# Optimization experiments

Hardware: AMD Instinct MI355X
Metric: run time of the kernel (lower is better)

The kernel has to match this reference:

```python
import jax, jax.numpy as jnp
import numpy as np

H, LMAX, NSEG, EPS = 8, 2, 16, 1e-7
S = (LMAX + 1) ** 2  # 9 spherical components
L_OF_M = jnp.asarray(np.floor(np.sqrt(np.arange(S))).astype(np.int32))  # degree l of each m-component


def so3_linear(x, W, b):
    # x [n,S,Cin]; W [LMAX+1,Cin,Cout] per-degree weights; bias only on l=0 (invariant) component
    y = jnp.einsum('nsi,sio->nso', x, W[L_OF_M])
    return y + b[None, None, :] * (jnp.arange(S) == 0)[None, :, None]


def equiv_layernorm(x, gamma, beta):
    # x [N,S,C]; standard LN on l=0 scalars, RMS-of-irrep-norm scaling (equivariant) for l>0
    x0 = x[:, 0, :]
    mu = jnp.mean(x0, -1, keepdims=True)
    var = jnp.mean((x0 - mu) ** 2, -1, keepdims=True)
    outs = [(((x0 - mu) / jnp.sqrt(var + EPS)) * gamma[0] + beta)[:, None, :]]
    for l in range(1, LMAX + 1):
        xl = x[:, l * l:(l + 1) * (l + 1), :]               # [N,2l+1,C]
        n2 = jnp.mean(xl * xl, axis=1)                      # [N,C] mean sq over m
        rms = jnp.sqrt(jnp.mean(n2, -1, keepdims=True) + EPS)  # [N,1]
        outs.append(xl / rms[:, None, :] * gamma[l][None, None, :])
    return jnp.concatenate(outs, axis=1)


def setup_inputs() -> dict:
    key = jax.random.key(0)
    ks = jax.random.split(key, 12)
    N, E, CIN, CH = 512, 8192, 128, 256
    return dict(
        q=jax.random.normal(ks[0], (N, S, CIN), jnp.float32),
        k=jax.random.normal(ks[1], (N, S, CIN), jnp.float32),
        v=jax.random.normal(ks[2], (N, S, CIN), jnp.float32),
        envelope=jax.random.uniform(ks[3], (E,), jnp.float32),
        attn_bias=jax.random.normal(ks[4], (H, E), jnp.float32),
        atom_index=jax.random.randint(ks[5], (E,), 0, N),
        batch_index=jnp.sort(jax.random.randint(ks[6], (E,), 0, NSEG)),
        edge_map_tab=jax.random.randint(ks[7], (E,), 0, E),
        Wq=jax.random.normal(ks[8], (LMAX + 1, CIN, CH), jnp.float32) / np.float32(np.sqrt(CIN)),
        bq=jnp.zeros((CH,), jnp.float32),
        Wk=jax.random.normal(ks[9], (LMAX + 1, CIN, CH), jnp.float32) / np.float32(np.sqrt(CIN)),
        bk=jnp.zeros((CH,), jnp.float32),
        Wv=jax.random.normal(ks[10], (LMAX + 1, CIN, CH), jnp.float32) / np.float32(np.sqrt(CIN)),
        bv=jnp.zeros((CH,), jnp.float32),
        gamma=jnp.ones((LMAX + 1, CH), jnp.float32),
        beta=jnp.zeros((CH,), jnp.float32),
        Wo=jax.random.normal(ks[11], (LMAX + 1, CH, CIN), jnp.float32) / np.float32(np.sqrt(CH)),
        bo=jnp.zeros((CIN,), jnp.float32),
    )


def reference(q, k, v, envelope, attn_bias, atom_index, batch_index, edge_map_tab,
              Wq, bq, Wk, bk, Wv, bv, gamma, beta, Wo, bo):
    N, E = q.shape[0], atom_index.shape[0]
    qh = so3_linear(q, Wq, bq)                      # [N,S,CH]
    kh = so3_linear(k, Wk, bk)[atom_index]          # [E,S,CH] gather per edge
    vh = so3_linear(v, Wv, bv)[atom_index]
    CH = qh.shape[-1]
    d = CH // H
    qh = qh.reshape(N, S, H, d).transpose(2, 0, 1, 3).reshape(H, N, S * d)
    kh = kh.reshape(E, S, H, d).transpose(2, 0, 1, 3).reshape(H, E, S * d)
    vh = vh.reshape(E, S, H, d).transpose(2, 0, 1, 3).reshape(H, E, S * d)
    scale = np.float32(np.sqrt(d / 3.0) / d)
    scores = jnp.einsum('hnf,hef->hne', qh * scale, kh)         # [H,N,E]
    scores = scores + attn_bias[:, edge_map_tab][:, None, :]
    env_e = envelope[edge_map_tab]                               # [E]
    # smooth scatter softmax grouped by batch_index over edge axis
    st = scores.transpose(2, 0, 1)                               # [E,H,N]
    mx = jax.ops.segment_max(st, batch_index, num_segments=NSEG)
    rec = jnp.exp(st - mx[batch_index]) * env_e[:, None, None]
    den = jax.ops.segment_sum(rec, batch_index, num_segments=NSEG)
    attn = rec / (den[batch_index] + 1e-16)
    attn = (attn * env_e[:, None, None]).transpose(1, 2, 0)      # [H,N,E]
    out = jnp.einsum('hne,hef->hnf', attn, vh)                   # [H,N,S*d]
    out = out.transpose(1, 0, 2).reshape(N, H, S, d).transpose(0, 2, 1, 3).reshape(N, S, CH)
    out = equiv_layernorm(out, gamma, beta)
    return so3_linear(out, Wo, bo)
```

## Files before the change

### kernel.cpp

```cpp
#include <hip/hip_runtime.h>
#include <hip/hip_bf16.h>
#include <math.h>

#define NH 8
#define SDIM 9
#define NSEG 16
#define NATOM 512
#define NEDGE 8192
#define CIN 128
#define CHN 256
#define DH 32
#define FDIM 288
#define EPS 1e-7f
#define SCALE 0.10206207261596577f

typedef __attribute__((ext_vector_type(8))) short bf16x8;
typedef __attribute__((ext_vector_type(8))) short short8;
typedef __attribute__((ext_vector_type(4))) float f32x4;

__device__ inline float blockReduceMax(float v, float* red) {
    #pragma unroll
    for (int off = 32; off; off >>= 1) v = fmaxf(v, __shfl_xor(v, off, 64));
    int lane = threadIdx.x & 63, wid = threadIdx.x >> 6;
    if (lane == 0) red[wid] = v;
    __syncthreads();
    v = fmaxf(fmaxf(red[0], red[1]), fmaxf(red[2], red[3]));
    __syncthreads();
    return v;
}
__device__ inline int lower_bound_batch(const int* __restrict__ b, int val) {
    int lo = 0, hi = NEDGE;
    while (lo < hi) {
        int mid = (lo + hi) >> 1;
        if (b[mid] < val) lo = mid + 1; else hi = mid;
    }
    return lo;
}
__device__ inline ushort f2bu(float x) {
    __hip_bfloat16 b = __float2bfloat16(x);
    return *(ushort*)&b;
}
__device__ inline float bu2f(ushort u) {
    unsigned int v = ((unsigned int)u) << 16;
    return *(float*)&v;
}

__global__ void __launch_bounds__(256) stage1(const int* __restrict__ batch,
                                              const int* __restrict__ am, const int* __restrict__ emap,
                                              const float* __restrict__ envelope,
                                              const float* __restrict__ attn_bias,
                                              float* __restrict__ E1, float* __restrict__ E2,
                                              const float* __restrict__ q, const float* __restrict__ k,
                                              const float* __restrict__ v,
                                              const float* __restrict__ Wq, const float* __restrict__ Wk,
                                              const float* __restrict__ Wv,
                                              const float* __restrict__ bq, const float* __restrict__ bk,
                                              const float* __restrict__ bv,
                                              ushort* __restrict__ qhB,
                                              ushort* __restrict__ khB,
                                              ushort* __restrict__ vhT,
                                              const float* __restrict__ Wo,
                                              ushort* __restrict__ WoT,
                                              float* __restrict__ stats) {
    const int bid = blockIdx.x;
    const int tid = threadIdx.x;
    if (bid < NSEG * NH) {
        const int seg = bid & (NSEG - 1), h = bid >> 4;
        __shared__ float e1[NATOM];
        __shared__ float e2[NATOM];
        __shared__ float red[4];
        e1[tid] = 0.f; e1[tid + 256] = 0.f;
        e2[tid] = 0.f; e2[tid + 256] = 0.f;
        const float* bh = attn_bias + (size_t)h * NEDGE;
        float mv = -1e30f;
        for (int e = tid; e < NEDGE; e += 256) mv = fmaxf(mv, bh[e]);
        const float mb = blockReduceMax(mv, red);
        const int st = lower_bound_batch(batch, seg);
        const int en = lower_bound_batch(batch, seg + 1);
        for (int e = st + tid; e < en; e += 256) {
            int m = am[e], em = emap[e];
            float ev = envelope[em];
            float eb = __expf(bh[em] - mb);
            atomicAdd(&e1[m], ev * eb);
            atomicAdd(&e2[m], ev * ev * eb);
        }
        __syncthreads();
        size_t base = ((size_t)h * NSEG + seg) * NATOM;
        E1[base + tid] = e1[tid]; E1[base + tid + 256] = e1[tid + 256];
        E2[base + tid] = e2[tid]; E2[base + tid + 256] = e2[tid + 256];
        return;
    }
    if (bid < NSEG * NH + 48) {
        const int t = bid - NSEG * NH;
        const int l = t / 16;
        const int cb = (t & 15) >> 2, ob = t & 3;
        const int c0 = cb * 64, o0 = ob * 32;
        __shared__ float tile[64][33];
        const float* src = Wo + (size_t)l * CHN * CIN;
        #pragma unroll
        for (int p = 0; p < 8; ++p) {
            int row = p * 8 + (tid >> 5);
            int col = tid & 31;
            tile[row][col] = src[(size_t)(c0 + row) * CIN + o0 + col];
        }
        __syncthreads();
        ushort* dst = WoT + (size_t)l * CIN * CHN;
        #pragma unroll
        for (int p = 0; p < 8; ++p) {
            int o = p * 4 + (tid >> 6);
            int c = tid & 63;
            dst[(size_t)(o0 + o) * CHN + c0 + c] = f2bu(tile[c][o]);
        }
        return;
    }
    if (bid < NSEG * NH + 48 + 432) {
        const int idx = bid - (NSEG * NH + 48);
        const int z = idx / 144;
        const int rem = idx - z * 144;
        const int s = rem >> 4;
        const int n0 = (rem & 15) * 32;
        const int l = (s == 0) ? 0 : ((s < 4) ? 1 : 2);
        const float* x = (z == 0) ? q : (z == 1) ? k : v;
        const float* W = ((z == 0) ? Wq : (z == 1) ? Wk : Wv) + (size_t)l * CIN * CHN;
        const float* bias = (z == 0) ? bq : (z == 1) ? bk : bv;
        const int lane = tid & 63, w = tid >> 6;
        const int wr = w >> 1, wc = w & 1;
        const int r = lane & 15, kg = lane >> 4;
        const int arow = n0 + 16 * wr + r;
        const float* xrow = x + ((size_t)arow * SDIM + s) * CIN;
        f32x4 acc[8] = {};
        #pragma unroll
        for (int ks = 0; ks < 4; ++ks) {
            const int k0 = ks * 32 + kg * 8;
            float4 x0 = *(const float4*)(xrow + k0);
            float4 x1 = *(const float4*)(xrow + k0 + 4);
            bf16x8 a;
            a[0] = f2bu(x0.x); a[1] = f2bu(x0.y); a[2] = f2bu(x0.z); a[3] = f2bu(x0.w);
            a[4] = f2bu(x1.x); a[5] = f2bu(x1.y); a[6] = f2bu(x1.z); a[7] = f2bu(x1.w);
            #pragma unroll
            for (int j = 0; j < 8; ++j) {
                const int o = 128 * wc + 16 * j + r;
                const float* wp = W + (size_t)k0 * CHN + o;
                bf16x8 bf;
                #pragma unroll
                for (int jj = 0; jj < 8; ++jj) bf[jj] = f2bu(wp[(size_t)jj * CHN]);
                acc[j] = __builtin_amdgcn_mfma_f32_16x16x32_bf16(a, bf, acc[j], 0, 0, 0);
            }
        }
        const float sc = (z == 0) ? SCALE : 1.0f;
        #pragma unroll
        for (int j = 0; j < 8; ++j) {
            const int o = 128 * wc + 16 * j + r;
            const float bb = (s == 0) ? bias[o] : 0.f;
            const int h = o >> 5, dj = o & 31;
            const int f = s * DH + dj;
            if (z < 2) {
                ushort* dst = (z == 0) ? qhB : khB;
                #pragma unroll
                for (int p = 0; p < 4; ++p) {
                    int row = n0 + 16 * wr + kg * 4 + p;
                    dst[((size_t)h * NATOM + row) * FDIM + f] = f2bu((acc[j][p] + bb) * sc);
                }
            } else {
                ushort* dst = vhT + ((size_t)h * FDIM + f) * NATOM;
                #pragma unroll
                for (int p = 0; p < 4; ++p) {
                    int row = n0 + 16 * wr + kg * 4 + p;
                    dst[row] = f2bu(acc[j][p] + bb);
                }
            }
        }
        return;
    }
    {
        float4 z4 = {0.f, 0.f, 0.f, 0.f};
        float4* sp = (float4*)stats;
        sp[tid] = z4;
        sp[tid + 256] = z4;
    }
}

#define SBST 520
__global__ void __launch_bounds__(512) attn_fused(const ushort* __restrict__ qhB,
                                                  const ushort* __restrict__ khB,
                                                  const float* __restrict__ E1,
                                                  const float* __restrict__ E2,
                                                  ushort* __restrict__ attnB) {
    const int h = blockIdx.x & 7;
    const int n0 = (blockIdx.x >> 3) * 16;
    __shared__ ushort sbuf[16 * SBST];
    __shared__ float rowmax[8][16];
    __shared__ float Dpart[8][16][NSEG];
    __shared__ float invDs[16][NSEG];
    const int tid = threadIdx.x;
    const int lane = tid & 63, w = tid >> 6;
    const int r = lane & 15, kg = lane >> 4;
    const ushort* A = qhB + (size_t)h * NATOM * FDIM;
    const ushort* B = khB + (size_t)h * NATOM * FDIM;
    const float* e1g = E1 + (size_t)h * NSEG * NATOM;
    const float* e2g = E2 + (size_t)h * NSEG * NATOM;
    const int ar = n0 + r;
    f32x4 acc[4] = {};
    #pragma unroll
    for (int ks = 0; ks < FDIM / 32; ++ks) {
        const int k0 = ks * 32 + kg * 8;
        bf16x8 a = *(const bf16x8*)(A + (size_t)ar * FDIM + k0);
        #pragma unroll
        for (int j = 0; j < 4; ++j) {
            const int bcol = w * 64 + 16 * j + r;
            bf16x8 b = *(const bf16x8*)(B + (size_t)bcol * FDIM + k0);
            acc[j] = __builtin_amdgcn_mfma_f32_16x16x32_bf16(a, b, acc[j], 0, 0, 0);
        }
    }
    float pm[4];
    #pragma unroll
    for (int p = 0; p < 4; ++p)
        pm[p] = fmaxf(fmaxf(acc[0][p], acc[1][p]), fmaxf(acc[2][p], acc[3][p]));
    #pragma unroll
    for (int mk = 1; mk < 16; mk <<= 1)
        #pragma unroll
        for (int p = 0; p < 4; ++p) pm[p] = fmaxf(pm[p], __shfl_xor(pm[p], mk, 64));
    if (r == 0) {
        #pragma unroll
        for (int p = 0; p < 4; ++p) rowmax[w][kg * 4 + p] = pm[p];
    }
    __syncthreads();
    float mx[4];
    #pragma unroll
    for (int p = 0; p < 4; ++p) {
        const int row = kg * 4 + p;
        float m = rowmax[0][row];
        #pragma unroll
        for (int ww2 = 1; ww2 < 8; ++ww2) m = fmaxf(m, rowmax[ww2][row]);
        mx[p] = m;
    }
    float es[4][4];
    #pragma unroll
    for (int j = 0; j < 4; ++j)
        #pragma unroll
        for (int p = 0; p < 4; ++p) es[j][p] = __expf(acc[j][p] - mx[p]);
    float Dp[4][NSEG] = {};
    #pragma unroll
    for (int j = 0; j < 4; ++j) {
        const int col = w * 64 + 16 * j + r;
        #pragma unroll
        for (int g = 0; g < NSEG; ++g) {
            float e1 = e1g[(size_t)g * NATOM + col];
            #pragma unroll
            for (int p = 0; p < 4; ++p) Dp[p][g] += es[j][p] * e1;
        }
    }
    #pragma unroll
    for (int mk = 1; mk < 16; mk <<= 1)
        #pragma unroll
        for (int p = 0; p < 4; ++p)
            #pragma unroll
            for (int g = 0; g < NSEG; ++g) Dp[p][g] += __shfl_xor(Dp[p][g], mk, 64);
    if (r == 0) {
        #pragma unroll
        for (int p = 0; p < 4; ++p)
            #pragma unroll
            for (int g = 0; g < NSEG; ++g) Dpart[w][kg * 4 + p][g] = Dp[p][g];
    }
    __syncthreads();
    if (tid < 256) {
        const int row = tid >> 4, g = tid & 15;
        float d = 0.f;
        #pragma unroll
        for (int ww2 = 0; ww2 < 8; ++ww2) d += Dpart[ww2][row][g];
        invDs[row][g] = 1.0f / (d + 1e-30f);
    }
    __syncthreads();
    float iv[4][NSEG];
    #pragma unroll
    for (int p = 0; p < 4; ++p)
        #pragma unroll
        for (int g = 0; g < NSEG; ++g) iv[p][g] = invDs[kg * 4 + p][g];
    #pragma unroll
    for (int j = 0; j < 4; ++j) {
        const int col = w * 64 + 16 * j + r;
        float ww[4] = {};
        #pragma unroll
        for (int g = 0; g < NSEG; ++g) {
            float e2 = e2g[(size_t)g * NATOM + col];
            #pragma unroll
            for (int p = 0; p < 4; ++p) ww[p] += e2 * iv[p][g];
        }
        #pragma unroll
        for (int p = 0; p < 4; ++p)
            sbuf[(kg * 4 + p) * SBST + col] = f2bu(es[j][p] * ww[p]);
    }
    __syncthreads();
    {
        ushort* dst = attnB + ((size_t)h * NATOM + n0) * NATOM;
        #pragma unroll
        for (int i = tid * 8; i < 16 * NATOM; i += 4096) {
            const int row = i >> 9, col = i & 511;
            *(short8*)(dst + (size_t)row * NATOM + col) = *(short8*)(sbuf + row * SBST + col);
        }
    }
}

__global__ void __launch_bounds__(256) gemm_out_stats(const ushort* __restrict__ attnB,
                                                      const ushort* __restrict__ vhT,
                                                      ushort* __restrict__ attnOutB,
                                                      float* __restrict__ stats) {
    const int h = blockIdx.x & 7;
    const int rest = blockIdx.x >> 3;
    const int fb = rest % 9;
    const int n0 = (rest / 9) * 64;
    const int tid = threadIdx.x;
    const int lane = tid & 63, w = tid >> 6;
    const int r = lane & 15, kg = lane >> 4;
    const ushort* A = attnB + (size_t)h * NATOM * NATOM;
    const ushort* B = vhT + (size_t)h * FDIM * NATOM;
    const int ar = n0 + 16 * w + r;
    f32x4 acc[2] = {};
    #pragma unroll 4
    for (int ks = 0; ks < NATOM / 32; ++ks) {
        const int k0 = ks * 32 + kg * 8;
        bf16x8 a = *(const bf16x8*)(A + (size_t)ar * NATOM + k0);
        bf16x8 b0 = *(const bf16x8*)(B + (size_t)(32 * fb + r) * NATOM + k0);
        bf16x8 b1 = *(const bf16x8*)(B + (size_t)(32 * fb + 16 + r) * NATOM + k0);
        acc[0] = __builtin_amdgcn_mfma_f32_16x16x32_bf16(a, b0, acc[0], 0, 0, 0);
        acc[1] = __builtin_amdgcn_mfma_f32_16x16x32_bf16(a, b1, acc[1], 0, 0, 0);
    }
    float sA[4], sB[4];
    #pragma unroll
    for (int p = 0; p < 4; ++p) { sA[p] = 0.f; sB[p] = 0.f; }
    #pragma unroll
    for (int j = 0; j < 2; ++j) {
        const int dj = 16 * j + r;
        #pragma unroll
        for (int p = 0; p < 4; ++p) {
            const int row = n0 + 16 * w + kg * 4 + p;
            float x = acc[j][p];
            attnOutB[((size_t)row * SDIM + fb) * CHN + h * DH + dj] = f2bu(x);
            sA[p] += x;
            sB[p] += x * x;
        }
    }
    #pragma unroll
    for (int mk = 1; mk < 16; mk <<= 1)
        #pragma unroll
        for (int p = 0; p < 4; ++p) {
            sA[p] += __shfl_xor(sA[p], mk, 64);
            sB[p] += __shfl_xor(sB[p], mk, 64);
        }
    if (r == 0) {
        #pragma unroll
        for (int p = 0; p < 4; ++p) {
            const int row = n0 + 16 * w + kg * 4 + p;
            if (fb == 0) {
                atomicAdd(&stats[row * 4 + 0], sA[p]);
                atomicAdd(&stats[row * 4 + 1], sB[p]);
            } else if (fb < 4) {
                atomicAdd(&stats[row * 4 + 2], sB[p]);
            } else {
                atomicAdd(&stats[row * 4 + 3], sB[p]);
            }
        }
    }
}

__global__ void __launch_bounds__(256) so3out_ln(const ushort* __restrict__ attnOutB,
                                                 const float* __restrict__ stats,
                                                 const float* __restrict__ gamma,
                                                 const float* __restrict__ beta,
                                                 const ushort* __restrict__ WoT,
                                                 const float* __restrict__ bo,
                                                 float* __restrict__ out) {
    const int s = blockIdx.y;
    const int n0 = blockIdx.x * 16;
    const int l = (s == 0) ? 0 : ((s < 4) ? 1 : 2);
    const int tid = threadIdx.x;
    const int lane = tid & 63, w = tid >> 6;
    const int r = lane & 15, kg = lane >> 4;
    const int ar = n0 + r;
    float mu, ivl;
    {
        float s0 = stats[ar * 4 + 0];
        float q0 = stats[ar * 4 + 1];
        float q1 = stats[ar * 4 + 2];
        float q2 = stats[ar * 4 + 3];
        float m0 = s0 * (1.0f / CHN);
        float var = q0 * (1.0f / CHN) - m0 * m0;
        if (s == 0) { mu = m0; ivl = 1.0f / sqrtf(var + EPS); }
        else if (s < 4) { mu = 0.f; ivl = 1.0f / sqrtf(q1 * (1.0f / (3 * CHN)) + EPS); }
        else { mu = 0.f; ivl = 1.0f / sqrtf(q2 * (1.0f / (5 * CHN)) + EPS); }
    }
    const ushort* xrow = attnOutB + ((size_t)ar * SDIM + s) * CHN;
    const float* gl = gamma + l * CHN;
    const ushort* B = WoT + (size_t)l * CIN * CHN;
    f32x4 acc[2] = {};
    #pragma unroll
    for (int ks = 0; ks < CHN / 32; ++ks) {
        const int k0 = ks * 32 + kg * 8;
        bf16x8 x8 = *(const bf16x8*)(xrow + k0);
        float4 g0 = *(const float4*)(gl + k0);
        float4 g1 = *(const float4*)(gl + k0 + 4);
        float y[8];
        y[0] = (bu2f((ushort)x8[0]) - mu) * ivl * g0.x;
        y[1] = (bu2f((ushort)x8[1]) - mu) * ivl * g0.y;
        y[2] = (bu2f((ushort)x8[2]) - mu) * ivl * g0.z;
        y[3] = (bu2f((ushort)x8[3]) - mu) * ivl * g0.w;
        y[4] = (bu2f((ushort)x8[4]) - mu) * ivl * g1.x;
        y[5] = (bu2f((ushort)x8[5]) - mu) * ivl * g1.y;
        y[6] = (bu2f((ushort)x8[6]) - mu) * ivl * g1.z;
        y[7] = (bu2f((ushort)x8[7]) - mu) * ivl * g1.w;
        if (s == 0) {
            float4 b0 = *(const float4*)(beta + k0);
            float4 b1 = *(const float4*)(beta + k0 + 4);
            y[0] += b0.x; y[1] += b0.y; y[2] += b0.z; y[3] += b0.w;
            y[4] += b1.x; y[5] += b1.y; y[6] += b1.z; y[7] += b1.w;
        }
        bf16x8 a;
        #pragma unroll
        for (int jj = 0; jj < 8; ++jj) a[jj] = f2bu(y[jj]);
        bf16x8 b0f = *(const bf16x8*)(B + (size_t)(32 * w + r) * CHN + k0);
        bf16x8 b1f = *(const bf16x8*)(B + (size_t)(32 * w + 16 + r) * CHN + k0);
        acc[0] = __builtin_amdgcn_mfma_f32_16x16x32_bf16(a, b0f, acc[0], 0, 0, 0);
        acc[1] = __builtin_amdgcn_mfma_f32_16x16x32_bf16(a, b1f, acc[1], 0, 0, 0);
    }
    #pragma unroll
    for (int j = 0; j < 2; ++j) {
        const int o = 32 * w + 16 * j + r;
        const float badd = (s == 0) ? bo[o] : 0.f;
        #pragma unroll
        for (int p = 0; p < 4; ++p) {
            const int n = n0 + kg * 4 + p;
            out[((size_t)n * SDIM + s) * CIN + o] = acc[j][p] + badd;
        }
    }
}

extern "C" void kernel_launch(void* const* d_in, const int* in_sizes, int n_in,
                              void* d_out, int out_size, void* d_ws, size_t ws_size,
                              hipStream_t stream) {
    const float* q = (const float*)d_in[0];
    const float* k = (const float*)d_in[1];
    const float* v = (const float*)d_in[2];
    const float* envelope = (const float*)d_in[3];
    const float* attn_bias = (const float*)d_in[4];
    const int* atom_index = (const int*)d_in[5];
    const int* batch_index = (const int*)d_in[6];
    const int* edge_map = (const int*)d_in[7];
    const float* Wq = (const float*)d_in[8];
    const float* bq = (const float*)d_in[9];
    const float* Wk = (const float*)d_in[10];
    const float* bk = (const float*)d_in[11];
    const float* Wv = (const float*)d_in[12];
    const float* bv = (const float*)d_in[13];
    const float* gamma = (const float*)d_in[14];
    const float* beta = (const float*)d_in[15];
    const float* Wo = (const float*)d_in[16];
    const float* bo = (const float*)d_in[17];
    float* out = (float*)d_out;

    const size_t SZ_HNF = (size_t)NH * NATOM * FDIM;
    const size_t SZ_HNN = (size_t)NH * NATOM * NATOM;
    const size_t SZ_TAB = (size_t)NH * NSEG * NATOM;
    const size_t SZ_WOT = (size_t)3 * CIN * CHN;
    const size_t SZ_NSC = (size_t)NATOM * SDIM * CHN;

    char* wsb = (char*)d_ws;
    ushort* qhB = (ushort*)wsb;
    ushort* khB = qhB + SZ_HNF;
    ushort* vhT = khB + SZ_HNF;
    ushort* attnB = vhT + SZ_HNF;
    ushort* attnOutB = attnB + SZ_HNN;
    float* E1 = (float*)(attnOutB + SZ_NSC);
    float* E2 = E1 + SZ_TAB;
    ushort* WoT = (ushort*)(E2 + SZ_TAB);
    float* stats = (float*)(WoT + SZ_WOT);

    size_t needed = 2 * (3 * SZ_HNF + SZ_HNN + SZ_NSC + SZ_WOT)
                  + 4 * 2 * SZ_TAB + 4 * NATOM * 4 + 256;
    if (ws_size < needed) return;

    stage1<<<NSEG * NH + 48 + 432 + 1, 256, 0, stream>>>(
        batch_index, atom_index, edge_map, envelope, attn_bias, E1, E2,
        q, k, v, Wq, Wk, Wv, bq, bk, bv, qhB, khB, vhT, Wo, WoT, stats);
    attn_fused<<<NATOM / 16 * NH, 512, 0, stream>>>(qhB, khB, E1, E2, attnB);
    gemm_out_stats<<<SDIM * (NATOM / 64) * NH, 256, 0, stream>>>(attnB, vhT, attnOutB, stats);
    so3out_ln<<<dim3(NATOM / 16, SDIM), 256, 0, stream>>>(
        attnOutB, stats, gamma, beta, WoT, bo, out);
}
```

Before: 72.75 us.

## Fuse all four stages into one persistent kernel with grid-wide barriers

Replaces the four separate launches (projection/edge tables, attention scores, attention·V GEMM with stats, layernorm+output projection) with a single persistent kernel of 256 blocks. Each stage loops over its original tile count, and stages are separated by atomic-counter grid barriers. A memset zeroes the stats and the barrier counter. This removes inter-kernel launch gaps and tail effects, but stages that previously used more blocks (or 512 threads) now run on fewer resident blocks, and the spin barriers depend on all 256 blocks being co-resident.

```diff
diff --git a/kernel.cpp b/kernel.cpp
--- a/kernel.cpp
+++ b/kernel.cpp
@@ -13,21 +13,13 @@
 #define FDIM 288
 #define EPS 1e-7f
 #define SCALE 0.10206207261596577f
+#define SBST 520
+#define GRID 256
 
 typedef __attribute__((ext_vector_type(8))) short bf16x8;
 typedef __attribute__((ext_vector_type(8))) short short8;
 typedef __attribute__((ext_vector_type(4))) float f32x4;
 
-__device__ inline float blockReduceMax(float v, float* red) {
-    #pragma unroll
-    for (int off = 32; off; off >>= 1) v = fmaxf(v, __shfl_xor(v, off, 64));
-    int lane = threadIdx.x & 63, wid = threadIdx.x >> 6;
-    if (lane == 0) red[wid] = v;
-    __syncthreads();
-    v = fmaxf(fmaxf(red[0], red[1]), fmaxf(red[2], red[3]));
-    __syncthreads();
-    return v;
-}
 __device__ inline int lower_bound_batch(const int* __restrict__ b, int val) {
     int lo = 0, hi = NEDGE;
     while (lo < hi) {
@@ -45,391 +37,391 @@
     return *(float*)&v;
 }
 
-__global__ void __launch_bounds__(256) stage1(const int* __restrict__ batch,
-                                              const int* __restrict__ am, const int* __restrict__ emap,
-                                              const float* __restrict__ envelope,
-                                              const float* __restrict__ attn_bias,
-                                              float* __restrict__ E1, float* __restrict__ E2,
-                                              const float* __restrict__ q, const float* __restrict__ k,
-                                              const float* __restrict__ v,
-                                              const float* __restrict__ Wq, const float* __restrict__ Wk,
-                                              const float* __restrict__ Wv,
-                                              const float* __restrict__ bq, const float* __restrict__ bk,
-                                              const float* __restrict__ bv,
-                                              ushort* __restrict__ qhB,
-                                              ushort* __restrict__ khB,
-                                              ushort* __restrict__ vhT,
-                                              const float* __restrict__ Wo,
-                                              ushort* __restrict__ WoT,
-                                              float* __restrict__ stats) {
+__device__ inline void gbar(int* cnt, int target) {
+    __syncthreads();
+    if (threadIdx.x == 0) {
+        __threadfence();
+        __hip_atomic_fetch_add(cnt, 1, __ATOMIC_ACQ_REL, __HIP_MEMORY_SCOPE_AGENT);
+        while (__hip_atomic_load(cnt, __ATOMIC_ACQUIRE, __HIP_MEMORY_SCOPE_AGENT) < target) {
+            __builtin_amdgcn_s_sleep(2);
+        }
+        __threadfence();
+    }
+    __syncthreads();
+}
+
+__global__ void __launch_bounds__(256) fused_all(
+        const int* __restrict__ batch, const int* __restrict__ am, const int* __restrict__ emap,
+        const float* __restrict__ envelope, const float* __restrict__ attn_bias,
+        float* __restrict__ E1, float* __restrict__ E2,
+        const float* __restrict__ q, const float* __restrict__ k, const float* __restrict__ v,
+        const float* __restrict__ Wq, const float* __restrict__ Wk, const float* __restrict__ Wv,
+        const float* __restrict__ bq, const float* __restrict__ bk, const float* __restrict__ bv,
+        ushort* __restrict__ qhB, ushort* __restrict__ khB, ushort* __restrict__ vhT,
+        const float* __restrict__ Wo, ushort* __restrict__ WoT, float* __restrict__ stats,
+        ushort* __restrict__ attnB, ushort* __restrict__ attnOutB,
+        const float* __restrict__ gamma, const float* __restrict__ beta,
+        const float* __restrict__ bo, float* __restrict__ out, int* __restrict__ cnt) {
+    __shared__ __align__(16) char smem[22016];
     const int bid = blockIdx.x;
     const int tid = threadIdx.x;
-    if (bid < NSEG * NH) {
-        const int seg = bid & (NSEG - 1), h = bid >> 4;
-        __shared__ float e1[NATOM];
-        __shared__ float e2[NATOM];
-        __shared__ float red[4];
-        e1[tid] = 0.f; e1[tid + 256] = 0.f;
-        e2[tid] = 0.f; e2[tid + 256] = 0.f;
-        const float* bh = attn_bias + (size_t)h * NEDGE;
-        float mv = -1e30f;
-        for (int e = tid; e < NEDGE; e += 256) mv = fmaxf(mv, bh[e]);
-        const float mb = blockReduceMax(mv, red);
-        const int st = lower_bound_batch(batch, seg);
-        const int en = lower_bound_batch(batch, seg + 1);
-        for (int e = st + tid; e < en; e += 256) {
-            int m = am[e], em = emap[e];
-            float ev = envelope[em];
-            float eb = __expf(bh[em] - mb);
-            atomicAdd(&e1[m], ev * eb);
-            atomicAdd(&e2[m], ev * ev * eb);
-        }
-        __syncthreads();
-        size_t base = ((size_t)h * NSEG + seg) * NATOM;
-        E1[base + tid] = e1[tid]; E1[base + tid + 256] = e1[tid + 256];
-        E2[base + tid] = e2[tid]; E2[base + tid + 256] = e2[tid + 256];
-        return;
-    }
-    if (bid < NSEG * NH + 48) {
-        const int t = bid - NSEG * NH;
-        const int l = t / 16;
-        const int cb = (t & 15) >> 2, ob = t & 3;
-        const int c0 = cb * 64, o0 = ob * 32;
-        __shared__ float tile[64][33];
-        const float* src = Wo + (size_t)l * CHN * CIN;
-        #pragma unroll
-        for (int p = 0; p < 8; ++p) {
-            int row = p * 8 + (tid >> 5);
-            int col = tid & 31;
-            tile[row][col] = src[(size_t)(c0 + row) * CIN + o0 + col];
-        }
-        __syncthreads();
-        ushort* dst = WoT + (size_t)l * CIN * CHN;
-        #pragma unroll
-        for (int p = 0; p < 8; ++p) {
-            int o = p * 4 + (tid >> 6);
-            int c = tid & 63;
-            dst[(size_t)(o0 + o) * CHN + c0 + c] = f2bu(tile[c][o]);
-        }
-        return;
-    }
-    if (bid < NSEG * NH + 48 + 432) {
-        const int idx = bid - (NSEG * NH + 48);
-        const int z = idx / 144;
-        const int rem = idx - z * 144;
-        const int s = rem >> 4;
-        const int n0 = (rem & 15) * 32;
-        const int l = (s == 0) ? 0 : ((s < 4) ? 1 : 2);
-        const float* x = (z == 0) ? q : (z == 1) ? k : v;
-        const float* W = ((z == 0) ? Wq : (z == 1) ? Wk : Wv) + (size_t)l * CIN * CHN;
-        const float* bias = (z == 0) ? bq : (z == 1) ? bk : bv;
-        const int lane = tid & 63, w = tid >> 6;
-        const int wr = w >> 1, wc = w & 1;
-        const int r = lane & 15, kg = lane >> 4;
-        const int arow = n0 + 16 * wr + r;
-        const float* xrow = x + ((size_t)arow * SDIM + s) * CIN;
-        f32x4 acc[8] = {};
-        #pragma unroll
-        for (int ks = 0; ks < 4; ++ks) {
-            const int k0 = ks * 32 + kg * 8;
-            float4 x0 = *(const float4*)(xrow + k0);
-            float4 x1 = *(const float4*)(xrow + k0 + 4);
-            bf16x8 a;
-            a[0] = f2bu(x0.x); a[1] = f2bu(x0.y); a[2] = f2bu(x0.z); a[3] = f2bu(x0.w);
-            a[4] = f2bu(x1.x); a[5] = f2bu(x1.y); a[6] = f2bu(x1.z); a[7] = f2bu(x1.w);
+
+    for (int t = bid; t < 608; t += GRID) {
+        if (t < NSEG * NH) {
+            float* e1 = (float*)smem;
+            float* e2 = e1 + NATOM;
+            float* red = e2 + NATOM;
+            const int seg = t & (NSEG - 1), h = t >> 4;
+            e1[tid] = 0.f; e1[tid + 256] = 0.f;
+            e2[tid] = 0.f; e2[tid + 256] = 0.f;
+            const float* bh = attn_bias + (size_t)h * NEDGE;
+            float mv = -1e30f;
+            for (int e = tid; e < NEDGE; e += 256) mv = fmaxf(mv, bh[e]);
+            #pragma unroll
+            for (int off = 32; off; off >>= 1) mv = fmaxf(mv, __shfl_xor(mv, off, 64));
+            {
+                int lane = tid & 63, wid = tid >> 6;
+                if (lane == 0) red[wid] = mv;
+            }
+            __syncthreads();
+            const float mb = fmaxf(fmaxf(red[0], red[1]), fmaxf(red[2], red[3]));
+            const int st = lower_bound_batch(batch, seg);
+            const int en = lower_bound_batch(batch, seg + 1);
+            for (int e = st + tid; e < en; e += 256) {
+                int m = am[e], em = emap[e];
+                float ev = envelope[em];
+                float eb = __expf(bh[em] - mb);
+                atomicAdd(&e1[m], ev * eb);
+                atomicAdd(&e2[m], ev * ev * eb);
+            }
+            __syncthreads();
+            size_t base = ((size_t)h * NSEG + seg) * NATOM;
+            E1[base + tid] = e1[tid]; E1[base + tid + 256] = e1[tid + 256];
+            E2[base + tid] = e2[tid]; E2[base + tid + 256] = e2[tid + 256];
+        } else if (t < NSEG * NH + 48) {
+            float (*tile)[33] = (float(*)[33])smem;
+            const int tt = t - NSEG * NH;
+            const int l = tt / 16;
+            const int cb = (tt & 15) >> 2, ob = tt & 3;
+            const int c0 = cb * 64, o0 = ob * 32;
+            const float* src = Wo + (size_t)l * CHN * CIN;
+            #pragma unroll
+            for (int p = 0; p < 8; ++p) {
+                int row = p * 8 + (tid >> 5);
+                int col = tid & 31;
+                tile[row][col] = src[(size_t)(c0 + row) * CIN + o0 + col];
+            }
+            __syncthreads();
+            ushort* dst = WoT + (size_t)l * CIN * CHN;
+            #pragma unroll
+            for (int p = 0; p < 8; ++p) {
+                int o = p * 4 + (tid >> 6);
+                int c = tid & 63;
+                dst[(size_t)(o0 + o) * CHN + c0 + c] = f2bu(tile[c][o]);
+            }
+        } else {
+            const int idx = t - (NSEG * NH + 48);
+            const int z = idx / 144;
+            const int rem = idx - z * 144;
+            const int s = rem >> 4;
+            const int n0 = (rem & 15) * 32;
+            const int l = (s == 0) ? 0 : ((s < 4) ? 1 : 2);
+            const float* x = (z == 0) ? q : (z == 1) ? k : v;
+            const float* W = ((z == 0) ? Wq : (z == 1) ? Wk : Wv) + (size_t)l * CIN * CHN;
+            const float* bias = (z == 0) ? bq : (z == 1) ? bk : bv;
+            const int lane = tid & 63, w = tid >> 6;
+            const int wr = w >> 1, wc = w & 1;
+            const int r = lane & 15, kg = lane >> 4;
+            const int arow = n0 + 16 * wr + r;
+            const float* xrow = x + ((size_t)arow * SDIM + s) * CIN;
+            f32x4 acc[8] = {};
+            #pragma unroll
+            for (int ks = 0; ks < 4; ++ks) {
+                const int k0 = ks * 32 + kg * 8;
+                float4 x0 = *(const float4*)(xrow + k0);
+                float4 x1 = *(const float4*)(xrow + k0 + 4);
+                bf16x8 a;
+                a[0] = f2bu(x0.x); a[1] = f2bu(x0.y); a[2] = f2bu(x0.z); a[3] = f2bu(x0.w);
+                a[4] = f2bu(x1.x); a[5] = f2bu(x1.y); a[6] = f2bu(x1.z); a[7] = f2bu(x1.w);
+                #pragma unroll
+                for (int j = 0; j < 8; ++j) {
+                    const int o = 128 * wc + 16 * j + r;
+                    const float* wp = W + (size_t)k0 * CHN + o;
+                    bf16x8 bf;
+                    #pragma unroll
+                    for (int jj = 0; jj < 8; ++jj) bf[jj] = f2bu(wp[(size_t)jj * CHN]);
+                    acc[j] = __builtin_amdgcn_mfma_f32_16x16x32_bf16(a, bf, acc[j], 0, 0, 0);
+                }
+            }
+            const float sc = (z == 0) ? SCALE : 1.0f;
             #pragma unroll
             for (int j = 0; j < 8; ++j) {
                 const int o = 128 * wc + 16 * j + r;
-                const float* wp = W + (size_t)k0 * CHN + o;
-                bf16x8 bf;
+                const float bb = (s == 0) ? bias[o] : 0.f;
+                const int h = o >> 5, dj = o & 31;
+                const int f = s * DH + dj;
+                if (z < 2) {
+                    ushort* dst = (z == 0) ? qhB : khB;
+                    #pragma unroll
+                    for (int p = 0; p < 4; ++p) {
+                        int row = n0 + 16 * wr + kg * 4 + p;
+                        dst[((size_t)h * NATOM + row) * FDIM + f] = f2bu((acc[j][p] + bb) * sc);
+                    }
+                } else {
+                    ushort* dst = vhT + ((size_t)h * FDIM + f) * NATOM;
+                    #pragma unroll
+                    for (int p = 0; p < 4; ++p) {
+                        int row = n0 + 16 * wr + kg * 4 + p;
+                        dst[row] = f2bu(acc[j][p] + bb);
+                    }
+                }
+            }
+        }
+        __syncthreads();
+    }
+
+    gbar(cnt, GRID);
+
+    {
+        const int h = bid & 7;
+        const int n0 = (bid >> 3) * 16;
+        ushort* sbuf = (ushort*)smem;
+        float* rowmaxS = (float*)(smem + 16640);
+        float* DpartS  = (float*)(smem + 16896);
+        float* invDsS  = (float*)(smem + 20992);
+        const int lane = tid & 63, w = tid >> 6;
+        const int r = lane & 15, kg = lane >> 4;
+        const ushort* A = qhB + (size_t)h * NATOM * FDIM;
+        const ushort* B = khB + (size_t)h * NATOM * FDIM;
+        const float* e1g = E1 + (size_t)h * NSEG * NATOM;
+        const float* e2g = E2 + (size_t)h * NSEG * NATOM;
+        const int ar = n0 + r;
+        f32x4 acc[8] = {};
+        #pragma unroll
+        for (int ks = 0; ks < FDIM / 32; ++ks) {
+            const int k0 = ks * 32 + kg * 8;
+            bf16x8 a = *(const bf16x8*)(A + (size_t)ar * FDIM + k0);
+            #pragma unroll
+            for (int j = 0; j < 8; ++j) {
+                const int bcol = w * 128 + 16 * j + r;
+                bf16x8 b = *(const bf16x8*)(B + (size_t)bcol * FDIM + k0);
+                acc[j] = __builtin_amdgcn_mfma_f32_16x16x32_bf16(a, b, acc[j], 0, 0, 0);
+            }
+        }
+        float pm[4];
+        #pragma unroll
+        for (int p = 0; p < 4; ++p) {
+            float m = acc[0][p];
+            #pragma unroll
+            for (int j = 1; j < 8; ++j) m = fmaxf(m, acc[j][p]);
+            pm[p] = m;
+        }
+        #pragma unroll
+        for (int mk = 1; mk < 16; mk <<= 1)
+            #pragma unroll
+            for (int p = 0; p < 4; ++p) pm[p] = fmaxf(pm[p], __shfl_xor(pm[p], mk, 64));
+        if (r == 0) {
+            #pragma unroll
+            for (int p = 0; p < 4; ++p) rowmaxS[w * 16 + kg * 4 + p] = pm[p];
+        }
+        __syncthreads();
+        float mx[4];
+        #pragma unroll
+        for (int p = 0; p < 4; ++p) {
+            const int row = kg * 4 + p;
+            mx[p] = fmaxf(fmaxf(rowmaxS[row], rowmaxS[16 + row]),
+                          fmaxf(rowmaxS[32 + row], rowmaxS[48 + row]));
+        }
+        float es[8][4];
+        #pragma unroll
+        for (int j = 0; j < 8; ++j)
+            #pragma unroll
+            for (int p = 0; p < 4; ++p) es[j][p] = __expf(acc[j][p] - mx[p]);
+        float Dp[4][NSEG] = {};
+        #pragma unroll
+        for (int j = 0; j < 8; ++j) {
+            const int col = w * 128 + 16 * j + r;
+            #pragma unroll
+            for (int g = 0; g < NSEG; ++g) {
+                float e1 = e1g[(size_t)g * NATOM + col];
                 #pragma unroll
-                for (int jj = 0; jj < 8; ++jj) bf[jj] = f2bu(wp[(size_t)jj * CHN]);
-                acc[j] = __builtin_amdgcn_mfma_f32_16x16x32_bf16(a, bf, acc[j], 0, 0, 0);
-            }
-        }
-        const float sc = (z == 0) ? SCALE : 1.0f;
+                for (int p = 0; p < 4; ++p) Dp[p][g] += es[j][p] * e1;
+            }
+        }
+        #pragma unroll
+        for (int mk = 1; mk < 16; mk <<= 1)
+            #pragma unroll
+            for (int p = 0; p < 4; ++p)
+                #pragma unroll
+                for (int g = 0; g < NSEG; ++g) Dp[p][g] += __shfl_xor(Dp[p][g], mk, 64);
+        if (r == 0) {
+            #pragma unroll
+            for (int p = 0; p < 4; ++p)
+                #pragma unroll
+                for (int g = 0; g < NSEG; ++g)
+                    DpartS[(w * 16 + kg * 4 + p) * 16 + g] = Dp[p][g];
+        }
+        __syncthreads();
+        {
+            const int row = tid >> 4, g = tid & 15;
+            float d = DpartS[row * 16 + g] + DpartS[(16 + row) * 16 + g]
+                    + DpartS[(32 + row) * 16 + g] + DpartS[(48 + row) * 16 + g];
+            invDsS[row * 16 + g] = 1.0f / (d + 1e-30f);
+        }
+        __syncthreads();
+        float iv[4][NSEG];
+        #pragma unroll
+        for (int p = 0; p < 4; ++p)
+            #pragma unroll
+            for (int g = 0; g < NSEG; ++g) iv[p][g] = invDsS[(kg * 4 + p) * 16 + g];
         #pragma unroll
         for (int j = 0; j < 8; ++j) {
-            const int o = 128 * wc + 16 * j + r;
-            const float bb = (s == 0) ? bias[o] : 0.f;
-            const int h = o >> 5, dj = o & 31;
-            const int f = s * DH + dj;
-            if (z < 2) {
-                ushort* dst = (z == 0) ? qhB : khB;
+            const int col = w * 128 + 16 * j + r;
+            float ww[4] = {};
+            #pragma unroll
+            for (int g = 0; g < NSEG; ++g) {
+                float e2 = e2g[(size_t)g * NATOM + col];
                 #pragma unroll
-                for (int p = 0; p < 4; ++p) {
-                    int row = n0 + 16 * wr + kg * 4 + p;
-                    dst[((size_t)h * NATOM + row) * FDIM + f] = f2bu((acc[j][p] + bb) * sc);
+                for (int p = 0; p < 4; ++p) ww[p] += e2 * iv[p][g];
+            }
+            #pragma unroll
+            for (int p = 0; p < 4; ++p)
+                sbuf[(kg * 4 + p) * SBST + col] = f2bu(es[j][p] * ww[p]);
+        }
+        __syncthreads();
+        {
+            ushort* dst = attnB + ((size_t)h * NATOM + n0) * NATOM;
+            #pragma unroll
+            for (int i = tid * 8; i < 16 * NATOM; i += 2048) {
+                const int row = i >> 9, col = i & 511;
+                *(short8*)(dst + (size_t)row * NATOM + col) = *(short8*)(sbuf + row * SBST + col);
+            }
+        }
+    }
+
+    gbar(cnt, 2 * GRID);
+
+    for (int t = bid; t < 576; t += GRID) {
+        const int h = t & 7;
+        const int rest = t >> 3;
+        const int fb = rest % 9;
+        const int n0 = (rest / 9) * 64;
+        const int lane = tid & 63, w = tid >> 6;
+        const int r = lane & 15, kg = lane >> 4;
+        const ushort* A = attnB + (size_t)h * NATOM * NATOM;
+        const ushort* B = vhT + (size_t)h * FDIM * NATOM;
+        const int ar = n0 + 16 * w + r;
+        f32x4 acc[2] = {};
+        #pragma unroll 4
+        for (int ks = 0; ks < NATOM / 32; ++ks) {
+            const int k0 = ks * 32 + kg * 8;
+            bf16x8 a = *(const bf16x8*)(A + (size_t)ar * NATOM + k0);
+            bf16x8 b0 = *(const bf16x8*)(B + (size_t)(32 * fb + r) * NATOM + k0);
+            bf16x8 b1 = *(const bf16x8*)(B + (size_t)(32 * fb + 16 + r) * NATOM + k0);
+            acc[0] = __builtin_amdgcn_mfma_f32_16x16x32_bf16(a, b0, acc[0], 0, 0, 0);
+            acc[1] = __builtin_amdgcn_mfma_f32_16x16x32_bf16(a, b1, acc[1], 0, 0, 0);
+        }
+        float sA[4], sB[4];
+        #pragma unroll
+        for (int p = 0; p < 4; ++p) { sA[p] = 0.f; sB[p] = 0.f; }
+        #pragma unroll
+        for (int j = 0; j < 2; ++j) {
+            const int dj = 16 * j + r;
+            #pragma unroll
+            for (int p = 0; p < 4; ++p) {
+                const int row = n0 + 16 * w + kg * 4 + p;
+                float x = acc[j][p];
+                attnOutB[((size_t)row * SDIM + fb) * CHN + h * DH + dj] = f2bu(x);
+                sA[p] += x;
+                sB[p] += x * x;
+            }
+        }
+        #pragma unroll
+        for (int mk = 1; mk < 16; mk <<= 1)
+            #pragma unroll
+            for (int p = 0; p < 4; ++p) {
+                sA[p] += __shfl_xor(sA[p], mk, 64);
+                sB[p] += __shfl_xor(sB[p], mk, 64);
+            }
+        if (r == 0) {
+            #pragma unroll
+            for (int p = 0; p < 4; ++p) {
+                const int row = n0 + 16 * w + kg * 4 + p;
+                if (fb == 0) {
+                    atomicAdd(&stats[row * 4 + 0], sA[p]);
+                    atomicAdd(&stats[row * 4 + 1], sB[p]);
+                } else if (fb < 4) {
+                    atomicAdd(&stats[row * 4 + 2], sB[p]);
+                } else {
+                    atomicAdd(&stats[row * 4 + 3], sB[p]);
                 }
-            } else {
-                ushort* dst = vhT + ((size_t)h * FDIM + f) * NATOM;
-                #pragma unroll
-                for (int p = 0; p < 4; ++p) {
-                    int row = n0 + 16 * wr + kg * 4 + p;
-                    dst[row] = f2bu(acc[j][p] + bb);
-                }
-            }
-        }
-        return;
-    }
-    {
-        float4 z4 = {0.f, 0.f, 0.f, 0.f};
-        float4* sp = (float4*)stats;
-        sp[tid] = z4;
-        sp[tid + 256] = z4;
-    }
-}
-
-#define SBST 520
-__global__ void __launch_bounds__(512) attn_fused(const ushort* __restrict__ qhB,
-                                                  const ushort* __restrict__ khB,
-                                                  const float* __restrict__ E1,
-                                                  const float* __restrict__ E2,
-                                                  ushort* __restrict__ attnB) {
-    const int h = blockIdx.x & 7;
-    const int n0 = (blockIdx.x >> 3) * 16;
-    __shared__ ushort sbuf[16 * SBST];
-    __shared__ float rowmax[8][16];
-    __shared__ float Dpart[8][16][NSEG];
-    __shared__ float invDs[16][NSEG];
-    const int tid = threadIdx.x;
-    const int lane = tid & 63, w = tid >> 6;
-    const int r = lane & 15, kg = lane >> 4;
-    const ushort* A = qhB + (size_t)h * NATOM * FDIM;
-    const ushort* B = khB + (size_t)h * NATOM * FDIM;
-    const float* e1g = E1 + (size_t)h * NSEG * NATOM;
-    const float* e2g = E2 + (size_t)h * NSEG * NATOM;
-    const int ar = n0 + r;
-    f32x4 acc[4] = {};
-    #pragma unroll
-    for (int ks = 0; ks < FDIM / 32; ++ks) {
-        const int k0 = ks * 32 + kg * 8;
-        bf16x8 a = *(const bf16x8*)(A + (size_t)ar * FDIM + k0);
-        #pragma unroll
-        for (int j = 0; j < 4; ++j) {
-            const int bcol = w * 64 + 16 * j + r;
-            bf16x8 b = *(const bf16x8*)(B + (size_t)bcol * FDIM + k0);
-            acc[j] = __builtin_amdgcn_mfma_f32_16x16x32_bf16(a, b, acc[j], 0, 0, 0);
-        }
-    }
-    float pm[4];
-    #pragma unroll
-    for (int p = 0; p < 4; ++p)
-        pm[p] = fmaxf(fmaxf(acc[0][p], acc[1][p]), fmaxf(acc[2][p], acc[3][p]));
-    #pragma unroll
-    for (int mk = 1; mk < 16; mk <<= 1)
-        #pragma unroll
-        for (int p = 0; p < 4; ++p) pm[p] = fmaxf(pm[p], __shfl_xor(pm[p], mk, 64));
-    if (r == 0) {
-        #pragma unroll
-        for (int p = 0; p < 4; ++p) rowmax[w][kg * 4 + p] = pm[p];
-    }
-    __syncthreads();
-    float mx[4];
-    #pragma unroll
-    for (int p = 0; p < 4; ++p) {
-        const int row = kg * 4 + p;
-        float m = rowmax[0][row];
-        #pragma unroll
-        for (int ww2 = 1; ww2 < 8; ++ww2) m = fmaxf(m, rowmax[ww2][row]);
-        mx[p] = m;
-    }
-    float es[4][4];
-    #pragma unroll
-    for (int j = 0; j < 4; ++j)
-        #pragma unroll
-        for (int p = 0; p < 4; ++p) es[j][p] = __expf(acc[j][p] - mx[p]);
-    float Dp[4][NSEG] = {};
-    #pragma unroll
-    for (int j = 0; j < 4; ++j) {
-        const int col = w * 64 + 16 * j + r;
-        #pragma unroll
-        for (int g = 0; g < NSEG; ++g) {
-            float e1 = e1g[(size_t)g * NATOM + col];
-            #pragma unroll
-            for (int p = 0; p < 4; ++p) Dp[p][g] += es[j][p] * e1;
-        }
-    }
-    #pragma unroll
-    for (int mk = 1; mk < 16; mk <<= 1)
-        #pragma unroll
-        for (int p = 0; p < 4; ++p)
-            #pragma unroll
-            for (int g = 0; g < NSEG; ++g) Dp[p][g] += __shfl_xor(Dp[p][g], mk, 64);
-    if (r == 0) {
-        #pragma unroll
-        for (int p = 0; p < 4; ++p)
-            #pragma unroll
-            for (int g = 0; g < NSEG; ++g) Dpart[w][kg * 4 + p][g] = Dp[p][g];
-    }
-    __syncthreads();
-    if (tid < 256) {
-        const int row = tid >> 4, g = tid & 15;
-        float d = 0.f;
-        #pragma unroll
-        for (int ww2 = 0; ww2 < 8; ++ww2) d += Dpart[ww2][row][g];
-        invDs[row][g] = 1.0f / (d + 1e-30f);
-    }
-    __syncthreads();
-    float iv[4][NSEG];
-    #pragma unroll
-    for (int p = 0; p < 4; ++p)
-        #pragma unroll
-        for (int g = 0; g < NSEG; ++g) iv[p][g] = invDs[kg * 4 + p][g];
-    #pragma unroll
-    for (int j = 0; j < 4; ++j) {
-        const int col = w * 64 + 16 * j + r;
-        float ww[4] = {};
-        #pragma unroll
-        for (int g = 0; g < NSEG; ++g) {
-            float e2 = e2g[(size_t)g * NATOM + col];
-            #pragma unroll
-            for (int p = 0; p < 4; ++p) ww[p] += e2 * iv[p][g];
-        }
-        #pragma unroll
-        for (int p = 0; p < 4; ++p)
-            sbuf[(kg * 4 + p) * SBST + col] = f2bu(es[j][p] * ww[p]);
-    }
-    __syncthreads();
-    {
-        ushort* dst = attnB + ((size_t)h * NATOM + n0) * NATOM;
-        #pragma unroll
-        for (int i = tid * 8; i < 16 * NATOM; i += 4096) {
-            const int row = i >> 9, col = i & 511;
-            *(short8*)(dst + (size_t)row * NATOM + col) = *(short8*)(sbuf + row * SBST + col);
-        }
-    }
-}
-
-__global__ void __launch_bounds__(256) gemm_out_stats(const ushort* __restrict__ attnB,
-                                                      const ushort* __restrict__ vhT,
-                                                      ushort* __restrict__ attnOutB,
-                                                      float* __restrict__ stats) {
-    const int h = blockIdx.x & 7;
-    const int rest = blockIdx.x >> 3;
-    const int fb = rest % 9;
-    const int n0 = (rest / 9) * 64;
-    const int tid = threadIdx.x;
-    const int lane = tid & 63, w = tid >> 6;
-    const int r = lane & 15, kg = lane >> 4;
-    const ushort* A = attnB + (size_t)h * NATOM * NATOM;
-    const ushort* B = vhT + (size_t)h * FDIM * NATOM;
-    const int ar = n0 + 16 * w + r;
-    f32x4 acc[2] = {};
-    #pragma unroll 4
-    for (int ks = 0; ks < NATOM / 32; ++ks) {
-        const int k0 = ks * 32 + kg * 8;
-        bf16x8 a = *(const bf16x8*)(A + (size_t)ar * NATOM + k0);
-        bf16x8 b0 = *(const bf16x8*)(B + (size_t)(32 * fb + r) * NATOM + k0);
-        bf16x8 b1 = *(const bf16x8*)(B + (size_t)(32 * fb + 16 + r) * NATOM + k0);
-        acc[0] = __builtin_amdgcn_mfma_f32_16x16x32_bf16(a, b0, acc[0], 0, 0, 0);
-        acc[1] = __builtin_amdgcn_mfma_f32_16x16x32_bf16(a, b1, acc[1], 0, 0, 0);
-    }
-    float sA[4], sB[4];
-    #pragma unroll
-    for (int p = 0; p < 4; ++p) { sA[p] = 0.f; sB[p] = 0.f; }
-    #pragma unroll
-    for (int j = 0; j < 2; ++j) {
-        const int dj = 16 * j + r;
-        #pragma unroll
-        for (int p = 0; p < 4; ++p) {
-            const int row = n0 + 16 * w + kg * 4 + p;
-            float x = acc[j][p];
-            attnOutB[((size_t)row * SDIM + fb) * CHN + h * DH + dj] = f2bu(x);
-            sA[p] += x;
-            sB[p] += x * x;
-        }
-    }
-    #pragma unroll
-    for (int mk = 1; mk < 16; mk <<= 1)
-        #pragma unroll
-        for (int p = 0; p < 4; ++p) {
-            sA[p] += __shfl_xor(sA[p], mk, 64);
-            sB[p] += __shfl_xor(sB[p], mk, 64);
-        }
-    if (r == 0) {
-        #pragma unroll
-        for (int p = 0; p < 4; ++p) {
-            const int row = n0 + 16 * w + kg * 4 + p;
-            if (fb == 0) {
-                atomicAdd(&stats[row * 4 + 0], sA[p]);
-                atomicAdd(&stats[row * 4 + 1], sB[p]);
-            } else if (fb < 4) {
-                atomicAdd(&stats[row * 4 + 2], sB[p]);
-            } else {
-                atomicAdd(&stats[row * 4 + 3], sB[p]);
-            }
-        }
-    }
-}
-
-__global__ void __launch_bounds__(256) so3out_ln(const ushort* __restrict__ attnOutB,
-                                                 const float* __restrict__ stats,
-                                                 const float* __restrict__ gamma,
-                                                 const float* __restrict__ beta,
-                                                 const ushort* __restrict__ WoT,
-                                                 const float* __restrict__ bo,
-                                                 float* __restrict__ out) {
-    const int s = blockIdx.y;
-    const int n0 = blockIdx.x * 16;
-    const int l = (s == 0) ? 0 : ((s < 4) ? 1 : 2);
-    const int tid = threadIdx.x;
-    const int lane = tid & 63, w = tid >> 6;
-    const int r = lane & 15, kg = lane >> 4;
-    const int ar = n0 + r;
-    float mu, ivl;
-    {
-        float s0 = stats[ar * 4 + 0];
-        float q0 = stats[ar * 4 + 1];
-        float q1 = stats[ar * 4 + 2];
-        float q2 = stats[ar * 4 + 3];
-        float m0 = s0 * (1.0f / CHN);
-        float var = q0 * (1.0f / CHN) - m0 * m0;
-        if (s == 0) { mu = m0; ivl = 1.0f / sqrtf(var + EPS); }
-        else if (s < 4) { mu = 0.f; ivl = 1.0f / sqrtf(q1 * (1.0f / (3 * CHN)) + EPS); }
-        else { mu = 0.f; ivl = 1.0f / sqrtf(q2 * (1.0f / (5 * CHN)) + EPS); }
-    }
-    const ushort* xrow = attnOutB + ((size_t)ar * SDIM + s) * CHN;
-    const float* gl = gamma + l * CHN;
-    const ushort* B = WoT + (size_t)l * CIN * CHN;
-    f32x4 acc[2] = {};
-    #pragma unroll
-    for (int ks = 0; ks < CHN / 32; ++ks) {
-        const int k0 = ks * 32 + kg * 8;
-        bf16x8 x8 = *(const bf16x8*)(xrow + k0);
-        float4 g0 = *(const float4*)(gl + k0);
-        float4 g1 = *(const float4*)(gl + k0 + 4);
-        float y[8];
-        y[0] = (bu2f((ushort)x8[0]) - mu) * ivl * g0.x;
-        y[1] = (bu2f((ushort)x8[1]) - mu) * ivl * g0.y;
-        y[2] = (bu2f((ushort)x8[2]) - mu) * ivl * g0.z;
-        y[3] = (bu2f((ushort)x8[3]) - mu) * ivl * g0.w;
-        y[4] = (bu2f((ushort)x8[4]) - mu) * ivl * g1.x;
-        y[5] = (bu2f((ushort)x8[5]) - mu) * ivl * g1.y;
-        y[6] = (bu2f((ushort)x8[6]) - mu) * ivl * g1.z;
-        y[7] = (bu2f((ushort)x8[7]) - mu) * ivl * g1.w;
-        if (s == 0) {
-            float4 b0 = *(const float4*)(beta + k0);
-            float4 b1 = *(const float4*)(beta + k0 + 4);
-            y[0] += b0.x; y[1] += b0.y; y[2] += b0.z; y[3] += b0.w;
-            y[4] += b1.x; y[5] += b1.y; y[6] += b1.z; y[7] += b1.w;
-        }
-        bf16x8 a;
-        #pragma unroll
-        for (int jj = 0; jj < 8; ++jj) a[jj] = f2bu(y[jj]);
-        bf16x8 b0f = *(const bf16x8*)(B + (size_t)(32 * w + r) * CHN + k0);
-        bf16x8 b1f = *(const bf16x8*)(B + (size_t)(32 * w + 16 + r) * CHN + k0);
-        acc[0] = __builtin_amdgcn_mfma_f32_16x16x32_bf16(a, b0f, acc[0], 0, 0, 0);
-        acc[1] = __builtin_amdgcn_mfma_f32_16x16x32_bf16(a, b1f, acc[1], 0, 0, 0);
-    }
-    #pragma unroll
-    for (int j = 0; j < 2; ++j) {
-        const int o = 32 * w + 16 * j + r;
-        const float badd = (s == 0) ? bo[o] : 0.f;
-        #pragma unroll
-        for (int p = 0; p < 4; ++p) {
-            const int n = n0 + kg * 4 + p;
-            out[((size_t)n * SDIM + s) * CIN + o] = acc[j][p] + badd;
+            }
+        }
+    }
+
+    gbar(cnt, 3 * GRID);
+
+    for (int t = bid; t < 288; t += GRID) {
+        const int s = t >> 5;
+        const int n0 = (t & 31) * 16;
+        const int l = (s == 0) ? 0 : ((s < 4) ? 1 : 2);
+        const int lane = tid & 63, w = tid >> 6;
+        const int r = lane & 15, kg = lane >> 4;
+        const int ar = n0 + r;
+        float mu, ivl;
+        {
+            float s0 = stats[ar * 4 + 0];
+            float q0 = stats[ar * 4 + 1];
+            float q1 = stats[ar * 4 + 2];
+            float q2 = stats[ar * 4 + 3];
+            float m0 = s0 * (1.0f / CHN);
+            float var = q0 * (1.0f / CHN) - m0 * m0;
+            if (s == 0) { mu = m0; ivl = 1.0f / sqrtf(var + EPS); }
+            else if (s < 4) { mu = 0.f; ivl = 1.0f / sqrtf(q1 * (1.0f / (3 * CHN)) + EPS); }
+            else { mu = 0.f; ivl = 1.0f / sqrtf(q2 * (1.0f / (5 * CHN)) + EPS); }
+        }
+        const ushort* xrow = attnOutB + ((size_t)ar * SDIM + s) * CHN;
+        const float* gl = gamma + l * CHN;
+        const ushort* B = WoT + (size_t)l * CIN * CHN;
+        f32x4 acc[2] = {};
+        #pragma unroll
+        for (int ks = 0; ks < CHN / 32; ++ks) {
+            const int k0 = ks * 32 + kg * 8;
+            bf16x8 x8 = *(const bf16x8*)(xrow + k0);
+            float4 g0 = *(const float4*)(gl + k0);
+            float4 g1 = *(const float4*)(gl + k0 + 4);
+            float y[8];
+            y[0] = (bu2f((ushort)x8[0]) - mu) * ivl * g0.x;
+            y[1] = (bu2f((ushort)x8[1]) - mu) * ivl * g0.y;
+            y[2] = (bu2f((ushort)x8[2]) - mu) * ivl * g0.z;
+            y[3] = (bu2f((ushort)x8[3]) - mu) * ivl * g0.w;
+            y[4] = (bu2f((ushort)x8[4]) - mu) * ivl * g1.x;
+            y[5] = (bu2f((ushort)x8[5]) - mu) * ivl * g1.y;
+            y[6] = (bu2f((ushort)x8[6]) - mu) * ivl * g1.z;
+            y[7] = (bu2f((ushort)x8[7]) - mu) * ivl * g1.w;
+            if (s == 0) {
+                float4 b0 = *(const float4*)(beta + k0);
+                float4 b1 = *(const float4*)(beta + k0 + 4);
+                y[0] += b0.x; y[1] += b0.y; y[2] += b0.z; y[3] += b0.w;
+                y[4] += b1.x; y[5] += b1.y; y[6] += b1.z; y[7] += b1.w;
+            }
+            bf16x8 a;
+            #pragma unroll
+            for (int jj = 0; jj < 8; ++jj) a[jj] = f2bu(y[jj]);
+            bf16x8 b0f = *(const bf16x8*)(B + (size_t)(32 * w + r) * CHN + k0);
+            bf16x8 b1f = *(const bf16x8*)(B + (size_t)(32 * w + 16 + r) * CHN + k0);
+            acc[0] = __builtin_amdgcn_mfma_f32_16x16x32_bf16(a, b0f, acc[0], 0, 0, 0);
+            acc[1] = __builtin_amdgcn_mfma_f32_16x16x32_bf16(a, b1f, acc[1], 0, 0, 0);
+        }
+        #pragma unroll
+        for (int j = 0; j < 2; ++j) {
+            const int o = 32 * w + 16 * j + r;
+            const float badd = (s == 0) ? bo[o] : 0.f;
+            #pragma unroll
+            for (int p = 0; p < 4; ++p) {
+                const int n = n0 + kg * 4 + p;
+                out[((size_t)n * SDIM + s) * CIN + o] = acc[j][p] + badd;
+            }
         }
     }
 }
@@ -478,11 +470,10 @@
                   + 4 * 2 * SZ_TAB + 4 * NATOM * 4 + 256;
     if (ws_size < needed) return;
 
-    stage1<<<NSEG * NH + 48 + 432 + 1, 256, 0, stream>>>(
+    int* cnt = (int*)(stats + NATOM * 4);
+    hipMemsetAsync(stats, 0, NATOM * 4 * sizeof(float) + 64, stream);
+    fused_all<<<GRID, 256, 0, stream>>>(
         batch_index, atom_index, edge_map, envelope, attn_bias, E1, E2,
-        q, k, v, Wq, Wk, Wv, bq, bk, bv, qhB, khB, vhT, Wo, WoT, stats);
-    attn_fused<<<NATOM / 16 * NH, 512, 0, stream>>>(qhB, khB, E1, E2, attnB);
-    gemm_out_stats<<<SDIM * (NATOM / 64) * NH, 256, 0, stream>>>(attnB, vhT, attnOutB, stats);
-    so3out_ln<<<dim3(NATOM / 16, SDIM), 256, 0, stream>>>(
-        attnOutB, stats, gamma, beta, WoT, bo, out);
-}
+        q, k, v, Wq, Wk, Wv, bq, bk, bv, qhB, khB, vhT, Wo, WoT, stats,
+        attnB, attnOutB, gamma, beta, bo, out, cnt);
+}
```

Result: slower. 211.3 us (+190.4%).
